# Kernel optimization log

Measured on AMD Instinct MI355X. Metric: run time of the kernel, lower is better.

The kernel has to match this reference:

```python
import jax, jax.numpy as jnp
import numpy as np

EPS = 1e-6

def layernorm2d(x, w, b):
    # normalize over channel dim (axis=1) of NCHW, per spatial location
    mu = jnp.mean(x, axis=1, keepdims=True)
    var = jnp.var(x, axis=1, keepdims=True)
    xn = (x - mu) * jax.lax.rsqrt(var + EPS)
    return xn * w[None, :, None, None] + b[None, :, None, None]

def conv1x1(x, w, b):
    # x: (B,C,H,W), w: (O,C), b: (O,)
    return jnp.einsum('bchw,oc->bohw', x, w) + b[None, :, None, None]

def setup_inputs() -> dict:
    key = jax.random.key(0)
    ks = jax.random.split(key, 9)
    B, C, H, W = 8, 256, 128, 128
    scale = 1.0 / np.sqrt(C)
    return {
        'x': jax.random.normal(ks[0], (B, C, H, W), jnp.float32),
        'norm_w': jnp.ones((C,), jnp.float32),
        'norm_b': jnp.zeros((C,), jnp.float32),
        'wq': jax.random.normal(ks[1], (C, C), jnp.float32) * scale,
        'bq': jnp.zeros((C,), jnp.float32),
        'wk': jax.random.normal(ks[2], (C, C), jnp.float32) * scale,
        'bk': jnp.zeros((C,), jnp.float32),
        'wv': jax.random.normal(ks[3], (C, C), jnp.float32) * scale,
        'bv': jnp.zeros((C,), jnp.float32),
        'beta': jax.random.normal(ks[4], (1, C, 1, 1), jnp.float32) * 0.1,
    }

def reference(x, norm_w, norm_b, wq, bq, wk, bk, wv, bv, beta):
    C = x.shape[1]
    scale = C ** (-0.5)
    xn = layernorm2d(x, norm_w, norm_b)
    Q = conv1x1(xn, wq, bq)          # (B,C,H,W)
    K = conv1x1(xn, wk, bk)          # (B,C,H,W)
    V = conv1x1(x, wv, bv)           # (B,C,H,W)
    # axial (per-row) attention: logits (B,H,W,W)
    attn = jnp.einsum('bchw,bchv->bhwv', Q, K) * scale
    A = jax.nn.softmax(attn, axis=-1)
    F_self = jnp.einsum('bhwv,bchv->bchw', A, V)
    return x + F_self * beta
```

## Files before the change

### kernel.cpp

```cpp
#include <hip/hip_runtime.h>
#include <hip/hip_bf16.h>

typedef short short8 __attribute__((ext_vector_type(8)));
typedef float f32x4 __attribute__((ext_vector_type(4)));

#define XN 0
#define AT 0
#define YTH 32768
#define GB 65536
#define SUMO 73728
#define SQO 75776
#define MUO 77824
#define RSO 78336
#define UDO 78848
#define LDS_BYTES 79360

__device__ inline unsigned short cvtbf(float f){
  unsigned int x = __float_as_uint(f);
  x += 0x7fffu + ((x >> 16) & 1u);
  return (unsigned short)(x >> 16);
}
__device__ inline float bf2f(unsigned short u){ return __uint_as_float(((unsigned int)u) << 16); }
__device__ inline unsigned int pk2(float a, float b){ return (unsigned int)cvtbf(a) | ((unsigned int)cvtbf(b) << 16); }

__global__ void __launch_bounds__(256) setup_kernel(
    const float* __restrict__ wq, const float* __restrict__ bq,
    const float* __restrict__ wk, const float* __restrict__ wvw,
    unsigned short* __restrict__ Mbf, unsigned short* __restrict__ wvbf, float* __restrict__ u){
  int t = threadIdx.x;
  int c1b = blockIdx.x * 4;
  float acc[4] = {0.f,0.f,0.f,0.f};
  for (int o = 0; o < 256; ++o){
    float wkv = wk[o*256 + t];
    #pragma unroll
    for (int i = 0; i < 4; ++i) acc[i] = fmaf(wq[o*256 + c1b + i], wkv, acc[i]);
  }
  #pragma unroll
  for (int i = 0; i < 4; ++i){
    Mbf[(c1b+i)*256 + t] = cvtbf(acc[i]);
    wvbf[(c1b+i)*256 + t] = cvtbf(wvw[(c1b+i)*256 + t]);
  }
  if (blockIdx.x == 0){
    float a2 = 0.f;
    for (int o = 0; o < 256; ++o) a2 = fmaf(wk[o*256 + t], bq[o], a2);
    u[t] = a2;
  }
}

__global__ void __launch_bounds__(512, 4) fused_kernel(
    const float* __restrict__ x, const float* __restrict__ nw, const float* __restrict__ nbp,
    const float* __restrict__ bvv, const float* __restrict__ beta,
    const unsigned short* __restrict__ Mbf, const unsigned short* __restrict__ wvbf,
    const float* __restrict__ u, float* __restrict__ out){
  extern __shared__ char smem[];
  const int t = threadIdx.x;
  const int lane = t & 63, wv8 = t >> 6;
  const int g = lane >> 4, li = lane & 15;
  const int blk = blockIdx.x;
  const int b = blk >> 7, h = blk & 127;
  const size_t base = (size_t)b*4194304 + (size_t)h*128;

  const int w = t & 127, s = t >> 7;
  unsigned int xp[32];
  {
    const float* xw = x + base + (size_t)(s*64)*16384 + w;
    float sm = 0.f, sq = 0.f;
    #pragma unroll
    for (int j = 0; j < 32; ++j){
      float a0 = xw[(size_t)(2*j)*16384];
      float a1 = xw[(size_t)(2*j+1)*16384];
      sm += a0 + a1;
      sq = fmaf(a0, a0, sq); sq = fmaf(a1, a1, sq);
      xp[j] = pk2(a0, a1);
    }
    ((float*)(smem + SUMO))[s*128 + w] = sm;
    ((float*)(smem + SQO))[s*128 + w] = sq;
  }
  __syncthreads();
  if (t < 128){
    float sm = 0.f, sq = 0.f;
    for (int q = 0; q < 4; ++q){ sm += ((float*)(smem+SUMO))[q*128+t]; sq += ((float*)(smem+SQO))[q*128+t]; }
    float mu = sm * (1.f/256.f);
    float var = sq * (1.f/256.f) - mu*mu;
    ((float*)(smem+MUO))[t] = mu;
    ((float*)(smem+RSO))[t] = rsqrtf(var + 1e-6f);
  }
  __syncthreads();

  {
    float mu = ((float*)(smem+MUO))[w], rs = ((float*)(smem+RSO))[w];
    float ud = 0.f;
    #pragma unroll
    for (int i = 0; i < 8; ++i){
      int c0 = s*64 + i*8;
      short8 o8;
      #pragma unroll
      for (int j = 0; j < 4; ++j){
        unsigned int p = xp[i*4 + j];
        int c = c0 + j*2;
        float xa = bf2f((unsigned short)(p & 0xffffu));
        float xb = bf2f((unsigned short)(p >> 16));
        float na = (xa - mu)*rs*nw[c]   + nbp[c];
        float nbv = (xb - mu)*rs*nw[c+1] + nbp[c+1];
        ud = fmaf(u[c], na, fmaf(u[c+1], nbv, ud));
        o8[j*2]   = (short)cvtbf(na);
        o8[j*2+1] = (short)cvtbf(nbv);
      }
      *(short8*)(smem + XN + w*512 + ((2*c0) ^ ((w&7)<<4))) = o8;
    }
    ((float*)(smem+SUMO))[s*128 + w] = ud;
  }
  __syncthreads();
  if (t < 128){
    float ud = 0.f; for (int q = 0; q < 4; ++q) ud += ((float*)(smem+SUMO))[q*128+t];
    ((float*)(smem+UDO))[t] = ud;
  }
  __syncthreads();

  f32x4 Sacc[8];
  #pragma unroll
  for (int vt = 0; vt < 8; ++vt){
    int vb = vt*16 + g*4;
    #pragma unroll
    for (int r = 0; r < 4; ++r) Sacc[vt][r] = ((float*)(smem+UDO))[vb + r];
  }
  const int ot = wv8 >> 2, vp = wv8 & 3;
  const int wt = wv8;
  for (int k8 = 0; k8 < 8; ++k8){
    f32x4 Ga[2] = {{0.f,0.f,0.f,0.f},{0.f,0.f,0.f,0.f}};
    #pragma unroll
    for (int kk = 0; kk < 8; ++kk){
      int o = k8*32 + ot*16 + li;
      short8 afr = *(const short8*)(Mbf + o*256 + kk*32 + g*8);
      #pragma unroll
      for (int j = 0; j < 2; ++j){
        int v = (vp*2 + j)*16 + li;
        short8 bfr = *(const short8*)(smem + XN + v*512 + ((2*(kk*32 + g*8)) ^ ((v&7)<<4)));
        Ga[j] = __builtin_amdgcn_mfma_f32_16x16x32_bf16(afr, bfr, Ga[j], 0, 0, 0);
      }
    }
    __syncthreads();
    #pragma unroll
    for (int j = 0; j < 2; ++j){
      int v = (vp*2 + j)*16 + li;
      int ob = ot*16 + g*4;
      uint2 p; p.x = pk2(Ga[j][0], Ga[j][1]); p.y = pk2(Ga[j][2], Ga[j][3]);
      *(uint2*)(smem + GB + v*64 + ((2*ob) ^ ((v&3)<<4))) = p;
    }
    __syncthreads();
    {
      int ww = wt*16 + li;
      short8 bfr = *(const short8*)(smem + XN + ww*512 + ((2*(k8*32 + g*8)) ^ ((ww&7)<<4)));
      #pragma unroll
      for (int vt = 0; vt < 8; ++vt){
        int v = vt*16 + li;
        short8 afr = *(const short8*)(smem + GB + v*64 + ((16*g) ^ ((v&3)<<4)));
        Sacc[vt] = __builtin_amdgcn_mfma_f32_16x16x32_bf16(afr, bfr, Sacc[vt], 0, 0, 0);
      }
    }
  }
  __syncthreads();

  float mx = -3.4e38f;
  #pragma unroll
  for (int vt = 0; vt < 8; ++vt)
    #pragma unroll
    for (int r = 0; r < 4; ++r){ float sv = Sacc[vt][r]*0.0625f; Sacc[vt][r] = sv; mx = fmaxf(mx, sv); }
  mx = fmaxf(mx, __shfl_xor(mx, 16));
  mx = fmaxf(mx, __shfl_xor(mx, 32));
  float sum = 0.f;
  #pragma unroll
  for (int vt = 0; vt < 8; ++vt)
    #pragma unroll
    for (int r = 0; r < 4; ++r){ float p = exp2f((Sacc[vt][r]-mx)*1.44269504f); Sacc[vt][r] = p; sum += p; }
  sum += __shfl_xor(sum, 16);
  sum += __shfl_xor(sum, 32);
  float inv = 1.f / sum;
  {
    int ww = wt*16 + li;
    #pragma unroll
    for (int vt = 0; vt < 8; ++vt){
      uint2 p; p.x = pk2(Sacc[vt][0]*inv, Sacc[vt][1]*inv); p.y = pk2(Sacc[vt][2]*inv, Sacc[vt][3]*inv);
      int vb = vt*16 + g*4;
      *(uint2*)(smem + AT + ww*256 + ((2*vb) ^ ((ww&7)<<4))) = p;
    }
  }
  __syncthreads();

  f32x4 Yacc[2][8];
  #pragma unroll
  for (int ci = 0; ci < 2; ++ci)
    #pragma unroll
    for (int w2 = 0; w2 < 8; ++w2) Yacc[ci][w2] = (f32x4){0.f,0.f,0.f,0.f};
  #pragma unroll
  for (int kk = 0; kk < 4; ++kk){
    short8 afr[2];
    #pragma unroll
    for (int ci = 0; ci < 2; ++ci){
      int c = (wv8*2 + ci)*16 + li;
      const float* xs = x + base + (size_t)c*16384 + (kk*32 + g*8);
      const float4 f0 = *(const float4*)xs;
      const float4 f1 = *(const float4*)(xs + 4);
      short8 a;
      a[0]=(short)cvtbf(f0.x); a[1]=(short)cvtbf(f0.y); a[2]=(short)cvtbf(f0.z); a[3]=(short)cvtbf(f0.w);
      a[4]=(short)cvtbf(f1.x); a[5]=(short)cvtbf(f1.y); a[6]=(short)cvtbf(f1.z); a[7]=(short)cvtbf(f1.w);
      afr[ci] = a;
    }
    #pragma unroll
    for (int w2 = 0; w2 < 8; ++w2){
      int ww = w2*16 + li;
      short8 bfr = *(const short8*)(smem + AT + ww*256 + ((2*(kk*32 + g*8)) ^ ((ww&7)<<4)));
      #pragma unroll
      for (int ci = 0; ci < 2; ++ci)
        Yacc[ci][w2] = __builtin_amdgcn_mfma_f32_16x16x32_bf16(afr[ci], bfr, Yacc[ci][w2], 0, 0, 0);
    }
  }

  f32x4 Facc[2][8];
  #pragma unroll
  for (int oi = 0; oi < 2; ++oi)
    #pragma unroll
    for (int w2 = 0; w2 < 8; ++w2) Facc[oi][w2] = (f32x4){0.f,0.f,0.f,0.f};
  for (int half = 0; half < 2; ++half){
    if ((wv8 >> 2) == half){
      #pragma unroll
      for (int ci = 0; ci < 2; ++ci){
        int cb = ((wv8 & 3)*2 + ci)*16 + g*4;
        #pragma unroll
        for (int w2 = 0; w2 < 8; ++w2){
          int ww = w2*16 + li;
          uint2 p; p.x = pk2(Yacc[ci][w2][0], Yacc[ci][w2][1]); p.y = pk2(Yacc[ci][w2][2], Yacc[ci][w2][3]);
          *(uint2*)(smem + YTH + ww*256 + ((2*cb) ^ ((ww&7)<<4))) = p;
        }
      }
    }
    __syncthreads();
    #pragma unroll
    for (int kk = 0; kk < 4; ++kk){
      short8 afr[2];
      #pragma unroll
      for (int oi = 0; oi < 2; ++oi){
        int o = (wv8*2 + oi)*16 + li;
        afr[oi] = *(const short8*)(wvbf + o*256 + half*128 + kk*32 + g*8);
      }
      #pragma unroll
      for (int w2 = 0; w2 < 8; ++w2){
        int ww = w2*16 + li;
        short8 bfr = *(const short8*)(smem + YTH + ww*256 + ((2*(kk*32 + g*8)) ^ ((ww&7)<<4)));
        #pragma unroll
        for (int oi = 0; oi < 2; ++oi)
          Facc[oi][w2] = __builtin_amdgcn_mfma_f32_16x16x32_bf16(afr[oi], bfr, Facc[oi][w2], 0, 0, 0);
      }
    }
    __syncthreads();
  }

  #pragma unroll
  for (int oi = 0; oi < 2; ++oi){
    #pragma unroll
    for (int r = 0; r < 4; ++r){
      int o = (wv8*2 + oi)*16 + g*4 + r;
      float bvo = bvv[o], bto = beta[o];
      #pragma unroll
      for (int w2 = 0; w2 < 8; ++w2){
        int ww = w2*16 + li;
        size_t idx = base + (size_t)o*16384 + (size_t)ww;
        out[idx] = x[idx] + (Facc[oi][w2][r] + bvo)*bto;
      }
    }
  }
}

extern "C" void kernel_launch(void* const* d_in, const int* in_sizes, int n_in,
                              void* d_out, int out_size, void* d_ws, size_t ws_size,
                              hipStream_t stream) {
  (void)in_sizes; (void)n_in; (void)out_size; (void)ws_size;
  const float* x      = (const float*)d_in[0];
  const float* norm_w = (const float*)d_in[1];
  const float* norm_b = (const float*)d_in[2];
  const float* wq     = (const float*)d_in[3];
  const float* bq     = (const float*)d_in[4];
  const float* wk     = (const float*)d_in[5];
  const float* wvw    = (const float*)d_in[7];
  const float* bvv    = (const float*)d_in[8];
  const float* beta   = (const float*)d_in[9];
  float* out = (float*)d_out;

  unsigned short* Mbf  = (unsigned short*)d_ws;
  unsigned short* wvbf = (unsigned short*)((char*)d_ws + 131072);
  float* u             = (float*)((char*)d_ws + 262144);

  static bool attr_set = false;
  if (!attr_set) {
    (void)hipFuncSetAttribute((const void*)fused_kernel,
                              hipFuncAttributeMaxDynamicSharedMemorySize, LDS_BYTES);
    attr_set = true;
  }

  setup_kernel<<<64, 256, 0, stream>>>(wq, bq, wk, wvw, Mbf, wvbf, u);
  fused_kernel<<<1024, 512, LDS_BYTES, stream>>>(x, norm_w, norm_b, bvv, beta, Mbf, wvbf, u, out);
}
```

Baseline: 235.5 us.

## Vectorize x loads, cache norm params in LDS, prefetch weights, add setprio

Changes the initial x load to float2 per thread over 32 channels, giving 8 partial-sum slices. LayerNorm weight, bias and u vectors are staged in LDS instead of read from global per element. The LDS swizzle masks are widened. Mbf fragments are software-prefetched one k8 iteration ahead, the x tiles for the Y GEMM are loaded before the softmax, and MFMA loops are wrapped in s_setprio. The prefetch buffers add register pressure, and the extra barrier and 8-way reductions add some synchronization.

```diff
diff --git a/kernel.cpp b/kernel.cpp
--- a/kernel.cpp
+++ b/kernel.cpp
@@ -8,12 +8,15 @@
 #define AT 0
 #define YTH 32768
 #define GB 65536
-#define SUMO 73728
-#define SQO 75776
-#define MUO 77824
-#define RSO 78336
-#define UDO 78848
-#define LDS_BYTES 79360
+#define SUMO 65536
+#define SQO 69632
+#define NW 73728
+#define NB 74752
+#define UU 75776
+#define MUO 76800
+#define RSO 77312
+#define UDO 77824
+#define LDS_BYTES 78336
 
 __device__ inline unsigned short cvtbf(float f){
   unsigned int x = __float_as_uint(f);
@@ -60,26 +63,34 @@
   const int b = blk >> 7, h = blk & 127;
   const size_t base = (size_t)b*4194304 + (size_t)h*128;
 
-  const int w = t & 127, s = t >> 7;
+  if (t < 256){
+    ((float*)(smem + NW))[t] = nw[t];
+    ((float*)(smem + NB))[t] = nbp[t];
+    ((float*)(smem + UU))[t] = u[t];
+  }
+
+  const int w2 = t & 63, s = t >> 6;
   unsigned int xp[32];
   {
-    const float* xw = x + base + (size_t)(s*64)*16384 + w;
-    float sm = 0.f, sq = 0.f;
+    const float* xw = x + base + (size_t)(s*32)*16384 + 2*w2;
+    float sm0 = 0.f, sq0 = 0.f, sm1 = 0.f, sq1 = 0.f;
     #pragma unroll
     for (int j = 0; j < 32; ++j){
-      float a0 = xw[(size_t)(2*j)*16384];
-      float a1 = xw[(size_t)(2*j+1)*16384];
-      sm += a0 + a1;
-      sq = fmaf(a0, a0, sq); sq = fmaf(a1, a1, sq);
-      xp[j] = pk2(a0, a1);
-    }
-    ((float*)(smem + SUMO))[s*128 + w] = sm;
-    ((float*)(smem + SQO))[s*128 + w] = sq;
+      float2 v = *(const float2*)(xw + (size_t)j*16384);
+      sm0 += v.x; sq0 = fmaf(v.x, v.x, sq0);
+      sm1 += v.y; sq1 = fmaf(v.y, v.y, sq1);
+      xp[j] = pk2(v.x, v.y);
+    }
+    ((float*)(smem + SUMO))[s*128 + 2*w2]     = sm0;
+    ((float*)(smem + SUMO))[s*128 + 2*w2 + 1] = sm1;
+    ((float*)(smem + SQO))[s*128 + 2*w2]      = sq0;
+    ((float*)(smem + SQO))[s*128 + 2*w2 + 1]  = sq1;
   }
   __syncthreads();
   if (t < 128){
     float sm = 0.f, sq = 0.f;
-    for (int q = 0; q < 4; ++q){ sm += ((float*)(smem+SUMO))[q*128+t]; sq += ((float*)(smem+SQO))[q*128+t]; }
+    #pragma unroll
+    for (int q = 0; q < 8; ++q){ sm += ((float*)(smem+SUMO))[q*128+t]; sq += ((float*)(smem+SQO))[q*128+t]; }
     float mu = sm * (1.f/256.f);
     float var = sq * (1.f/256.f) - mu*mu;
     ((float*)(smem+MUO))[t] = mu;
@@ -88,31 +99,36 @@
   __syncthreads();
 
   {
-    float mu = ((float*)(smem+MUO))[w], rs = ((float*)(smem+RSO))[w];
+    float ud[2] = {0.f, 0.f};
+    #pragma unroll
+    for (int r = 0; r < 2; ++r){
+      int w = 2*w2 + r;
+      float mu = ((float*)(smem+MUO))[w], rs = ((float*)(smem+RSO))[w];
+      #pragma unroll
+      for (int i = 0; i < 4; ++i){
+        int c0 = s*32 + i*8;
+        short8 o8;
+        #pragma unroll
+        for (int j = 0; j < 8; ++j){
+          int c = c0 + j;
+          unsigned int p = xp[i*8 + j];
+          float xv = bf2f((unsigned short)(r ? (p >> 16) : (p & 0xffffu)));
+          float nv = (xv - mu)*rs*((float*)(smem+NW))[c] + ((float*)(smem+NB))[c];
+          ud[r] = fmaf(((float*)(smem+UU))[c], nv, ud[r]);
+          o8[j] = (short)cvtbf(nv);
+        }
+        *(short8*)(smem + XN + w*512 + ((2*c0) ^ ((w&31)<<4))) = o8;
+      }
+    }
+    __syncthreads();
+    ((float*)(smem+SUMO))[s*128 + 2*w2]     = ud[0];
+    ((float*)(smem+SUMO))[s*128 + 2*w2 + 1] = ud[1];
+  }
+  __syncthreads();
+  if (t < 128){
     float ud = 0.f;
     #pragma unroll
-    for (int i = 0; i < 8; ++i){
-      int c0 = s*64 + i*8;
-      short8 o8;
-      #pragma unroll
-      for (int j = 0; j < 4; ++j){
-        unsigned int p = xp[i*4 + j];
-        int c = c0 + j*2;
-        float xa = bf2f((unsigned short)(p & 0xffffu));
-        float xb = bf2f((unsigned short)(p >> 16));
-        float na = (xa - mu)*rs*nw[c]   + nbp[c];
-        float nbv = (xb - mu)*rs*nw[c+1] + nbp[c+1];
-        ud = fmaf(u[c], na, fmaf(u[c+1], nbv, ud));
-        o8[j*2]   = (short)cvtbf(na);
-        o8[j*2+1] = (short)cvtbf(nbv);
-      }
-      *(short8*)(smem + XN + w*512 + ((2*c0) ^ ((w&7)<<4))) = o8;
-    }
-    ((float*)(smem+SUMO))[s*128 + w] = ud;
-  }
-  __syncthreads();
-  if (t < 128){
-    float ud = 0.f; for (int q = 0; q < 4; ++q) ud += ((float*)(smem+SUMO))[q*128+t];
+    for (int q = 0; q < 8; ++q) ud += ((float*)(smem+SUMO))[q*128+t];
     ((float*)(smem+UDO))[t] = ud;
   }
   __syncthreads();
@@ -126,19 +142,33 @@
   }
   const int ot = wv8 >> 2, vp = wv8 & 3;
   const int wt = wv8;
+  short8 mpre[4];
+  #pragma unroll
+  for (int kk = 0; kk < 4; ++kk)
+    mpre[kk] = *(const short8*)(Mbf + (ot*16 + li)*256 + kk*32 + g*8);
+  #pragma unroll
   for (int k8 = 0; k8 < 8; ++k8){
     f32x4 Ga[2] = {{0.f,0.f,0.f,0.f},{0.f,0.f,0.f,0.f}};
+    const int o = k8*32 + ot*16 + li;
+    short8 mnext[4];
+    __builtin_amdgcn_s_setprio(1);
     #pragma unroll
     for (int kk = 0; kk < 8; ++kk){
-      int o = k8*32 + ot*16 + li;
-      short8 afr = *(const short8*)(Mbf + o*256 + kk*32 + g*8);
+      short8 afr = (kk < 4) ? mpre[kk]
+                 : *(const short8*)(Mbf + o*256 + kk*32 + g*8);
+      if (kk < 4 && k8 < 7){
+        mnext[kk] = *(const short8*)(Mbf + ((k8+1)*32 + ot*16 + li)*256 + kk*32 + g*8);
+      }
       #pragma unroll
       for (int j = 0; j < 2; ++j){
         int v = (vp*2 + j)*16 + li;
-        short8 bfr = *(const short8*)(smem + XN + v*512 + ((2*(kk*32 + g*8)) ^ ((v&7)<<4)));
+        short8 bfr = *(const short8*)(smem + XN + v*512 + ((2*(kk*32 + g*8)) ^ ((v&31)<<4)));
         Ga[j] = __builtin_amdgcn_mfma_f32_16x16x32_bf16(afr, bfr, Ga[j], 0, 0, 0);
       }
     }
+    __builtin_amdgcn_s_setprio(0);
+    #pragma unroll
+    for (int kk = 0; kk < 4; ++kk) mpre[kk] = mnext[kk];
     __syncthreads();
     #pragma unroll
     for (int j = 0; j < 2; ++j){
@@ -150,16 +180,29 @@
     __syncthreads();
     {
       int ww = wt*16 + li;
-      short8 bfr = *(const short8*)(smem + XN + ww*512 + ((2*(k8*32 + g*8)) ^ ((ww&7)<<4)));
+      short8 bfr = *(const short8*)(smem + XN + ww*512 + ((2*(k8*32 + g*8)) ^ ((ww&31)<<4)));
+      __builtin_amdgcn_s_setprio(1);
       #pragma unroll
       for (int vt = 0; vt < 8; ++vt){
         int v = vt*16 + li;
         short8 afr = *(const short8*)(smem + GB + v*64 + ((16*g) ^ ((v&3)<<4)));
         Sacc[vt] = __builtin_amdgcn_mfma_f32_16x16x32_bf16(afr, bfr, Sacc[vt], 0, 0, 0);
       }
-    }
-  }
-  __syncthreads();
+      __builtin_amdgcn_s_setprio(0);
+    }
+  }
+  __syncthreads();
+
+  float4 xe[2][2][2];
+  #pragma unroll
+  for (int kb = 0; kb < 2; ++kb)
+    #pragma unroll
+    for (int ci = 0; ci < 2; ++ci){
+      int c = (wv8*2 + ci)*16 + li;
+      const float* xs = x + base + (size_t)c*16384 + (kb*32 + g*8);
+      xe[kb][ci][0] = *(const float4*)xs;
+      xe[kb][ci][1] = *(const float4*)(xs + 4);
+    }
 
   float mx = -3.4e38f;
   #pragma unroll
@@ -182,7 +225,7 @@
     for (int vt = 0; vt < 8; ++vt){
       uint2 p; p.x = pk2(Sacc[vt][0]*inv, Sacc[vt][1]*inv); p.y = pk2(Sacc[vt][2]*inv, Sacc[vt][3]*inv);
       int vb = vt*16 + g*4;
-      *(uint2*)(smem + AT + ww*256 + ((2*vb) ^ ((ww&7)<<4))) = p;
+      *(uint2*)(smem + AT + ww*256 + ((2*vb) ^ ((ww&15)<<4))) = p;
     }
   }
   __syncthreads();
@@ -191,46 +234,56 @@
   #pragma unroll
   for (int ci = 0; ci < 2; ++ci)
     #pragma unroll
-    for (int w2 = 0; w2 < 8; ++w2) Yacc[ci][w2] = (f32x4){0.f,0.f,0.f,0.f};
+    for (int w2i = 0; w2i < 8; ++w2i) Yacc[ci][w2i] = (f32x4){0.f,0.f,0.f,0.f};
   #pragma unroll
   for (int kk = 0; kk < 4; ++kk){
     short8 afr[2];
     #pragma unroll
     for (int ci = 0; ci < 2; ++ci){
-      int c = (wv8*2 + ci)*16 + li;
-      const float* xs = x + base + (size_t)c*16384 + (kk*32 + g*8);
-      const float4 f0 = *(const float4*)xs;
-      const float4 f1 = *(const float4*)(xs + 4);
+      const float4 f0 = xe[kk&1][ci][0];
+      const float4 f1 = xe[kk&1][ci][1];
       short8 a;
       a[0]=(short)cvtbf(f0.x); a[1]=(short)cvtbf(f0.y); a[2]=(short)cvtbf(f0.z); a[3]=(short)cvtbf(f0.w);
       a[4]=(short)cvtbf(f1.x); a[5]=(short)cvtbf(f1.y); a[6]=(short)cvtbf(f1.z); a[7]=(short)cvtbf(f1.w);
       afr[ci] = a;
     }
-    #pragma unroll
-    for (int w2 = 0; w2 < 8; ++w2){
-      int ww = w2*16 + li;
-      short8 bfr = *(const short8*)(smem + AT + ww*256 + ((2*(kk*32 + g*8)) ^ ((ww&7)<<4)));
+    if (kk < 2){
+      #pragma unroll
+      for (int ci = 0; ci < 2; ++ci){
+        int c = (wv8*2 + ci)*16 + li;
+        const float* xs = x + base + (size_t)c*16384 + ((kk+2)*32 + g*8);
+        xe[kk&1][ci][0] = *(const float4*)xs;
+        xe[kk&1][ci][1] = *(const float4*)(xs + 4);
+      }
+    }
+    __builtin_amdgcn_s_setprio(1);
+    #pragma unroll
+    for (int w2i = 0; w2i < 8; ++w2i){
+      int ww = w2i*16 + li;
+      short8 bfr = *(const short8*)(smem + AT + ww*256 + ((2*(kk*32 + g*8)) ^ ((ww&15)<<4)));
       #pragma unroll
       for (int ci = 0; ci < 2; ++ci)
-        Yacc[ci][w2] = __builtin_amdgcn_mfma_f32_16x16x32_bf16(afr[ci], bfr, Yacc[ci][w2], 0, 0, 0);
-    }
+        Yacc[ci][w2i] = __builtin_amdgcn_mfma_f32_16x16x32_bf16(afr[ci], bfr, Yacc[ci][w2i], 0, 0, 0);
+    }
+    __builtin_amdgcn_s_setprio(0);
   }
 
   f32x4 Facc[2][8];
   #pragma unroll
   for (int oi = 0; oi < 2; ++oi)
     #pragma unroll
-    for (int w2 = 0; w2 < 8; ++w2) Facc[oi][w2] = (f32x4){0.f,0.f,0.f,0.f};
+    for (int w2i = 0; w2i < 8; ++w2i) Facc[oi][w2i] = (f32x4){0.f,0.f,0.f,0.f};
+  #pragma unroll
   for (int half = 0; half < 2; ++half){
     if ((wv8 >> 2) == half){
       #pragma unroll
       for (int ci = 0; ci < 2; ++ci){
         int cb = ((wv8 & 3)*2 + ci)*16 + g*4;
         #pragma unroll
-        for (int w2 = 0; w2 < 8; ++w2){
-          int ww = w2*16 + li;
-          uint2 p; p.x = pk2(Yacc[ci][w2][0], Yacc[ci][w2][1]); p.y = pk2(Yacc[ci][w2][2], Yacc[ci][w2][3]);
-          *(uint2*)(smem + YTH + ww*256 + ((2*cb) ^ ((ww&7)<<4))) = p;
+        for (int w2i = 0; w2i < 8; ++w2i){
+          int ww = w2i*16 + li;
+          uint2 p; p.x = pk2(Yacc[ci][w2i][0], Yacc[ci][w2i][1]); p.y = pk2(Yacc[ci][w2i][2], Yacc[ci][w2i][3]);
+          *(uint2*)(smem + YTH + ww*256 + ((2*cb) ^ ((ww&15)<<4))) = p;
         }
       }
     }
@@ -243,14 +296,16 @@
         int o = (wv8*2 + oi)*16 + li;
         afr[oi] = *(const short8*)(wvbf + o*256 + half*128 + kk*32 + g*8);
       }
-      #pragma unroll
-      for (int w2 = 0; w2 < 8; ++w2){
-        int ww = w2*16 + li;
-        short8 bfr = *(const short8*)(smem + YTH + ww*256 + ((2*(kk*32 + g*8)) ^ ((ww&7)<<4)));
+      __builtin_amdgcn_s_setprio(1);
+      #pragma unroll
+      for (int w2i = 0; w2i < 8; ++w2i){
+        int ww = w2i*16 + li;
+        short8 bfr = *(const short8*)(smem + YTH + ww*256 + ((2*(kk*32 + g*8)) ^ ((ww&15)<<4)));
         #pragma unroll
         for (int oi = 0; oi < 2; ++oi)
-          Facc[oi][w2] = __builtin_amdgcn_mfma_f32_16x16x32_bf16(afr[oi], bfr, Facc[oi][w2], 0, 0, 0);
-      }
+          Facc[oi][w2i] = __builtin_amdgcn_mfma_f32_16x16x32_bf16(afr[oi], bfr, Facc[oi][w2i], 0, 0, 0);
+      }
+      __builtin_amdgcn_s_setprio(0);
     }
     __syncthreads();
   }
@@ -262,10 +317,10 @@
       int o = (wv8*2 + oi)*16 + g*4 + r;
       float bvo = bvv[o], bto = beta[o];
       #pragma unroll
-      for (int w2 = 0; w2 < 8; ++w2){
-        int ww = w2*16 + li;
+      for (int w2i = 0; w2i < 8; ++w2i){
+        int ww = w2i*16 + li;
         size_t idx = base + (size_t)o*16384 + (size_t)ww;
-        out[idx] = x[idx] + (Facc[oi][w2][r] + bvo)*bto;
+        out[idx] = x[idx] + (Facc[oi][w2i][r] + bvo)*bto;
       }
     }
   }
```

Result: faster. 209.4 us (-11.1%).
